# Kernel tuning notes

Measured on AMD Instinct MI355X. Metric: run time of the kernel, lower is better.

## Reference

```python
import jax, jax.numpy as jnp
import numpy as np
from jax import lax

EPS_BN = 1e-5
EPS_ADD = 1e-12


def _bn2d(x, g, b):
    # train-mode BatchNorm2d: stats over (N,H,W), biased variance
    m = x.mean(axis=(0, 2, 3), keepdims=True)
    v = x.var(axis=(0, 2, 3), keepdims=True)
    return (x - m) * lax.rsqrt(v + EPS_BN) * g[None, :, None, None] + b[None, :, None, None]


def _bn1d(x, g, b):
    # train-mode BatchNorm1d on [B,C,L]: stats over (N,L)
    m = x.mean(axis=(0, 2), keepdims=True)
    v = x.var(axis=(0, 2), keepdims=True)
    return (x - m) * lax.rsqrt(v + EPS_BN) * g[None, :, None] + b[None, :, None]


def _addw(w, a, b):
    wr = jax.nn.relu(w)
    wn = wr / (wr.sum() + EPS_ADD)
    return wn[0] * a + wn[1] * b


def setup_inputs() -> dict:
    key = jax.random.key(0)
    B, C, L = 16, 128, 16384
    H = 8
    ks = jax.random.split(key, 16)
    inp = {
        "x": jax.random.normal(ks[0], (B, C, L), dtype=jnp.float32),
        "dw_w": jax.random.normal(ks[1], (3, C, 1, 3, 3), dtype=jnp.float32) * 0.1,
        "bn2_g": jnp.ones((3, C), jnp.float32),
        "bn2_b": jnp.zeros((3, C), jnp.float32),
        "pw_w": jax.random.normal(ks[2], (3, C, C), dtype=jnp.float32) * 0.05,
        "pw_b": jax.random.normal(ks[3], (3, C), dtype=jnp.float32) * 0.02,
        "add_w": jnp.ones((2,), jnp.float32),
        "bn1_g": jnp.ones((C,), jnp.float32),
        "bn1_b": jnp.zeros((C,), jnp.float32),
        "W1": jax.random.normal(ks[4], (C, C // 4), dtype=jnp.float32) * 0.05,
        "b1": jnp.zeros((C // 4,), jnp.float32),
        "W2": jax.random.normal(ks[5], (C // 4, C), dtype=jnp.float32) * 0.05,
        "b2": jnp.zeros((C,), jnp.float32),
        "ffn_add_w": jnp.ones((2,), jnp.float32),
        "ffn_bn_g": jnp.ones((C,), jnp.float32),
        "ffn_bn_b": jnp.zeros((C,), jnp.float32),
        "heads": 8,
    }
    return inp


def reference(x, dw_w, bn2_g, bn2_b, pw_w, pw_b, add_w, bn1_g, bn1_b,
              W1, b1, W2, b2, ffn_add_w, ffn_bn_g, ffn_bn_b, heads):
    B, C, L = x.shape
    S = int(np.sqrt(L))  # static perfect-square side
    maps = x.reshape(B, C, S, S)

    # q (stride 1), k, v (stride 2) branches: depthwise3x3 -> BN2d -> pointwise1x1 -> GELU
    outs = []
    for i, st in enumerate((1, 2, 2)):
        y = lax.conv_general_dilated(
            maps, dw_w[i], window_strides=(st, st), padding=[(1, 1), (1, 1)],
            feature_group_count=C, dimension_numbers=("NCHW", "OIHW", "NCHW"))
        y = _bn2d(y, bn2_g[i], bn2_b[i])
        y = jnp.einsum("oc,bchw->bohw", pw_w[i], y) + pw_b[i][None, :, None, None]
        outs.append(jax.nn.gelu(y, approximate=False))
    q, k, v = outs

    def flat(t):  # [B,C,h,w] -> [B, n, C]
        return t.reshape(t.shape[0], t.shape[1], -1).transpose(0, 2, 1)

    q, k, v = flat(q), flat(k), flat(v)  # q: [B,L,C]; k,v: [B,L/4,C]
    dh = C // heads
    qh = q.reshape(B, -1, heads, dh)
    kh = k.reshape(B, -1, heads, dh)
    vh = v.reshape(B, -1, heads, dh)
    qs = jax.nn.softmax(qh, axis=-1)      # softmax over per-head channel dim
    ks_ = jax.nn.softmax(kh, axis=1)      # softmax over key sequence dim
    kv = jnp.einsum("bnhd,bnhe->bhde", ks_, vh)   # [B,H,dh,dh] tiny
    att = jnp.einsum("blhd,bhde->blhe", qs, kv)   # [B,L,H,dh]
    mhlsa = att.transpose(0, 2, 3, 1).reshape(B, C, L)  # concat heads on channel

    att_out = _bn1d(_addw(add_w, mhlsa, x), bn1_g, bn1_b)  # [B,C,L]

    # FFN on [B,L,C]
    f = jax.nn.gelu(jnp.einsum("blc,cf->blf", att_out.transpose(0, 2, 1), W1) + b1, approximate=False)
    f = jax.nn.gelu(jnp.einsum("blf,fc->blc", f, W2) + b2, approximate=False)
    out = _bn1d(_addw(ffn_add_w, f.transpose(0, 2, 1), att_out), ffn_bn_g, ffn_bn_b)
    return out
```

## Files before the change

kernel.cpp:

```cpp
#include <hip/hip_runtime.h>
#include <hip/hip_bf16.h>
#include <math.h>

#define BB 16
#define CC 128
#define LL 16384
#define SS 128
#define LK 4096
#define NHEAD 8
#define DH 16

typedef __attribute__((ext_vector_type(8))) short short8;
typedef __attribute__((ext_vector_type(4))) float f32x4;

__device__ __forceinline__ float gelu_f(float x) {
    return 0.5f * x * (1.0f + erff(x * 0.70710678118654752f));
}

__device__ __forceinline__ ushort f2bf(float f) {
    __hip_bfloat16 h = __float2bfloat16(f);
    return *(ushort*)&h;
}
__device__ __forceinline__ float bf2f(ushort u) {
    union { unsigned int i; float f; } x; x.i = ((unsigned int)u) << 16; return x.f;
}

__device__ __forceinline__ void block_reduce2(float& s1, float& s2) {
    #pragma unroll
    for (int off = 32; off; off >>= 1) {
        s1 += __shfl_down(s1, off);
        s2 += __shfl_down(s2, off);
    }
    __shared__ float red[2][4];
    int wid = threadIdx.x >> 6, lid = threadIdx.x & 63;
    if (lid == 0) { red[0][wid] = s1; red[1][wid] = s2; }
    __syncthreads();
    if (threadIdx.x == 0) {
        int nw = blockDim.x >> 6;
        float a = 0.f, b = 0.f;
        for (int i = 0; i < nw; i++) { a += red[0][i]; b += red[1][i]; }
        s1 = a; s2 = b;
    }
}

__global__ __launch_bounds__(256) void k_dw(const float* __restrict__ x,
        const float* __restrict__ dw_w,
        ushort* __restrict__ dwq, ushort* __restrict__ dwk, ushort* __restrict__ dwv,
        float* __restrict__ dwstats) {
    int bx = blockIdx.x;
    int cg = bx & 3;
    int oh = (bx >> 2) & 127;
    int b  = bx >> 9;
    __shared__ float xs[3][32][132];
    int tid = threadIdx.x;
    int cl  = tid >> 3;
    int owg = tid & 7;
    int ow0 = owg * 16;
    int c   = cg * 32 + cl;
    bool do_kv = ((oh & 1) == 0);

    float wq[9], wk[9], wv[9];
    const float* wp = dw_w + (size_t)c * 9;
    #pragma unroll
    for (int t = 0; t < 9; t++) wq[t] = wp[t];
    #pragma unroll
    for (int t = 0; t < 9; t++) wk[t] = wp[(size_t)CC * 9 + t];
    #pragma unroll
    for (int t = 0; t < 9; t++) wv[t] = wp[(size_t)2 * CC * 9 + t];

    for (int i = tid; i < 3 * 32 * 32; i += 256) {
        int r = i >> 10;
        int rem = i & 1023;
        int ch = rem >> 5;
        int f4 = rem & 31;
        int ih = oh - 1 + r;
        float4 v = make_float4(0.f, 0.f, 0.f, 0.f);
        if (ih >= 0 && ih < 128)
            v = *(const float4*)(x + ((size_t)b * CC + cg * 32 + ch) * (size_t)LL + ih * SS + f4 * 4);
        *(float4*)&xs[r][ch][f4 * 4] = v;
    }
    if (tid < 96) {
        int r = tid >> 5, ch = tid & 31;
        *(float4*)&xs[r][ch][128] = make_float4(0.f, 0.f, 0.f, 0.f);
    }
    __syncthreads();

    float aq[16], ak[8], av[8];
    #pragma unroll
    for (int j = 0; j < 16; j++) aq[j] = 0.f;
    #pragma unroll
    for (int j = 0; j < 8; j++) { ak[j] = 0.f; av[j] = 0.f; }

    #pragma unroll
    for (int r = 0; r < 3; r++) {
        const float* row = &xs[r][cl][0];
        float g[18];
        g[0] = owg ? row[ow0 - 1] : 0.f;
        float4 v0 = *(const float4*)&row[ow0];
        float4 v1 = *(const float4*)&row[ow0 + 4];
        float4 v2 = *(const float4*)&row[ow0 + 8];
        float4 v3 = *(const float4*)&row[ow0 + 12];
        g[1] = v0.x;  g[2] = v0.y;  g[3] = v0.z;  g[4] = v0.w;
        g[5] = v1.x;  g[6] = v1.y;  g[7] = v1.z;  g[8] = v1.w;
        g[9] = v2.x;  g[10] = v2.y; g[11] = v2.z; g[12] = v2.w;
        g[13] = v3.x; g[14] = v3.y; g[15] = v3.z; g[16] = v3.w;
        g[17] = row[ow0 + 16];
        float w0 = wq[3 * r], w1 = wq[3 * r + 1], w2 = wq[3 * r + 2];
        #pragma unroll
        for (int j = 0; j < 16; j++)
            aq[j] += w0 * g[j] + w1 * g[j + 1] + w2 * g[j + 2];
        if (do_kv) {
            float k0 = wk[3 * r], k1 = wk[3 * r + 1], k2 = wk[3 * r + 2];
            float x0 = wv[3 * r], x1 = wv[3 * r + 1], x2 = wv[3 * r + 2];
            #pragma unroll
            for (int j = 0; j < 8; j++) {
                ak[j] += k0 * g[2 * j] + k1 * g[2 * j + 1] + k2 * g[2 * j + 2];
                av[j] += x0 * g[2 * j] + x1 * g[2 * j + 1] + x2 * g[2 * j + 2];
            }
        }
    }

    ushort qb[16], kb16[8], vb16[8];
    {
        float s1 = 0.f, s2 = 0.f;
        #pragma unroll
        for (int j = 0; j < 16; j++) {
            qb[j] = f2bf(aq[j]);
            float fv = bf2f(qb[j]);
            s1 += fv; s2 += fv * fv;
        }
        #pragma unroll
        for (int m = 1; m <= 4; m <<= 1) {
            s1 += __shfl_xor(s1, m);
            s2 += __shfl_xor(s2, m);
        }
        if (owg == 0) {
            atomicAdd(&dwstats[(size_t)c * 2 + 0], s1);
            atomicAdd(&dwstats[(size_t)c * 2 + 1], s2);
        }
    }
    if (do_kv) {
        float t1 = 0.f, t2 = 0.f, u1 = 0.f, u2 = 0.f;
        #pragma unroll
        for (int j = 0; j < 8; j++) {
            kb16[j] = f2bf(ak[j]);
            float fk = bf2f(kb16[j]);
            t1 += fk; t2 += fk * fk;
            vb16[j] = f2bf(av[j]);
            float fv = bf2f(vb16[j]);
            u1 += fv; u2 += fv * fv;
        }
        #pragma unroll
        for (int m = 1; m <= 4; m <<= 1) {
            t1 += __shfl_xor(t1, m); t2 += __shfl_xor(t2, m);
            u1 += __shfl_xor(u1, m); u2 += __shfl_xor(u2, m);
        }
        if (owg == 0) {
            atomicAdd(&dwstats[((size_t)CC + c) * 2 + 0], t1);
            atomicAdd(&dwstats[((size_t)CC + c) * 2 + 1], t2);
            atomicAdd(&dwstats[((size_t)2 * CC + c) * 2 + 0], u1);
            atomicAdd(&dwstats[((size_t)2 * CC + c) * 2 + 1], u2);
        }
    }

    __syncthreads();
    unsigned int* qt = (unsigned int*)&xs[0][0][0];
    unsigned int* kt = qt + 64 * 33;
    unsigned int* vt = kt + 32 * 33;
    #pragma unroll
    for (int jp = 0; jp < 8; jp++)
        qt[(owg * 8 + jp) * 33 + cl] = (unsigned int)qb[2 * jp] | ((unsigned int)qb[2 * jp + 1] << 16);
    if (do_kv) {
        #pragma unroll
        for (int jp = 0; jp < 4; jp++) {
            kt[(owg * 4 + jp) * 33 + cl] = (unsigned int)kb16[2 * jp] | ((unsigned int)kb16[2 * jp + 1] << 16);
            vt[(owg * 4 + jp) * 33 + cl] = (unsigned int)vb16[2 * jp] | ((unsigned int)vb16[2 * jp + 1] << 16);
        }
    }
    __syncthreads();
    {
        ushort* qrow = dwq + (((size_t)b * 4 + cg) * LL + (size_t)oh * 128) * 32;
        #pragma unroll
        for (int cc = 0; cc < 2; cc++) {
            int i = tid + cc * 256;
            int p = i >> 2, c8 = (i & 3) * 8;
            int half = (p & 1) * 16;
            const unsigned int* src = qt + (p >> 1) * 33 + c8;
            union { ushort u[8]; float4 v; } pk;
            #pragma unroll
            for (int t2 = 0; t2 < 8; t2++) pk.u[t2] = (ushort)(src[t2] >> half);
            *(float4*)(qrow + (size_t)p * 32 + c8) = pk.v;
        }
    }
    if (do_kv) {
        int ohp = oh >> 1;
        size_t kvoff = (((size_t)b * 4 + cg) * LK + (size_t)ohp * 64) * 32;
        int p = tid >> 2, c8 = (tid & 3) * 8;
        int half = (p & 1) * 16;
        {
            const unsigned int* src = kt + (p >> 1) * 33 + c8;
            union { ushort u[8]; float4 v; } pk;
            #pragma unroll
            for (int t2 = 0; t2 < 8; t2++) pk.u[t2] = (ushort)(src[t2] >> half);
            *(float4*)(dwk + kvoff + (size_t)p * 32 + c8) = pk.v;
        }
        {
            const unsigned int* src = vt + (p >> 1) * 33 + c8;
            union { ushort u[8]; float4 v; } pk;
            #pragma unroll
            for (int t2 = 0; t2 < 8; t2++) pk.u[t2] = (ushort)(src[t2] >> half);
            *(float4*)(dwv + kvoff + (size_t)p * 32 + c8) = pk.v;
        }
    }
}

__global__ void k_finalize_dw(const float* __restrict__ stats, const float* __restrict__ pw_w,
                              const float* __restrict__ pw_b, const float* __restrict__ bn2_g,
                              const float* __restrict__ bn2_b,
                              ushort* __restrict__ effWb, float* __restrict__ effB) {
    int br = blockIdx.x >> 7;
    int o  = blockIdx.x & 127;
    int c  = threadIdx.x;
    float N = (br == 0) ? 262144.f : 65536.f;
    float s1 = stats[(br * CC + c) * 2 + 0];
    float s2 = stats[(br * CC + c) * 2 + 1];
    float m = s1 / N;
    float v = s2 / N - m * m;
    float sc = rsqrtf(v + 1e-5f);
    float A  = bn2_g[br * CC + c] * sc;
    float Bc = bn2_b[br * CC + c] - m * A;
    float w  = pw_w[((size_t)br * CC + o) * CC + c];
    effWb[((size_t)br * CC + o) * CC + c] = f2bf(w * A);
    float pb = w * Bc, dummy = 0.f;
    block_reduce2(pb, dummy);
    if (threadIdx.x == 0) effB[br * CC + o] = pw_b[br * CC + o] + pb;
}

__global__ __launch_bounds__(256, 3) void k_gemm_kv(const ushort* __restrict__ dwk,
        const ushort* __restrict__ dwv, const ushort* __restrict__ effWb,
        const float* __restrict__ effB, float* __restrict__ kbuf, float* __restrict__ vbuf) {
    __shared__ __align__(16) char raw[34816];
    short* Bs = (short*)raw;
    float* Sf = (float*)raw;
    int bx = blockIdx.x;
    int brv = bx >> 9;
    int b = (bx >> 5) & 15;
    int p0 = (bx & 31) * 128;
    const ushort* dw = brv ? dwv : dwk;
    const ushort* Wg = effWb + (size_t)(1 + brv) * CC * CC;
    int tid = threadIdx.x;
    for (int i = tid; i < 2048; i += 256) {
        int row = i >> 4; int f4 = i & 15;
        float4 v = *(const float4*)(Wg + (size_t)row * 128 + f4 * 8);
        *(float4*)&Bs[row * 136 + f4 * 8] = v;
    }
    __syncthreads();
    int w = tid >> 6, l = tid & 63;
    int m0 = w * 16;
    int la = l & 15, lb = l >> 4;
    f32x4 acc[2][8];
    #pragma unroll
    for (int i = 0; i < 2; i++)
        #pragma unroll
        for (int j = 0; j < 8; j++) acc[i][j] = (f32x4){0.f, 0.f, 0.f, 0.f};
    #pragma unroll
    for (int kt = 0; kt < 4; kt++) {
        short8 a0 = *(const short8*)(dw + (((size_t)b * 4 + kt) * LK + p0 + m0 + la) * 32 + lb * 8);
        short8 a1 = *(const short8*)(dw + (((size_t)b * 4 + kt) * LK + p0 + m0 + 64 + la) * 32 + lb * 8);
        int kb = kt * 32 + lb * 8;
        #pragma unroll
        for (int nt = 0; nt < 8; nt++) {
            short8 bf = *(const short8*)&Bs[(nt * 16 + la) * 136 + kb];
            acc[0][nt] = __builtin_amdgcn_mfma_f32_16x16x32_bf16(a0, bf, acc[0][nt], 0, 0, 0);
            acc[1][nt] = __builtin_amdgcn_mfma_f32_16x16x32_bf16(a1, bf, acc[1][nt], 0, 0, 0);
        }
    }
    float bias[8];
    #pragma unroll
    for (int nt = 0; nt < 8; nt++) bias[nt] = effB[(1 + brv) * CC + nt * 16 + la];
    float* outb = (brv ? vbuf : kbuf) + ((size_t)b * LK + p0) * CC;
    #pragma unroll
    for (int t = 0; t < 2; t++) {
        __syncthreads();
        #pragma unroll
        for (int nt = 0; nt < 8; nt++)
            #pragma unroll
            for (int i = 0; i < 4; i++) {
                float vv = acc[t][nt][i] + bias[nt];
                Sf[(m0 + lb * 4 + i) * 132 + nt * 16 + la] = gelu_f(vv);
            }
        __syncthreads();
        for (int i = tid; i < 2048; i += 256) {
            int r = i >> 5; int c4 = i & 31;
            *(float4*)(outb + (size_t)(t * 64 + r) * CC + c4 * 4) = *(const float4*)&Sf[r * 132 + c4 * 4];
        }
    }
}

__global__ void k_kv_accum(const float* __restrict__ k_buf, const float* __restrict__ v_buf,
                           float* __restrict__ kv_un, float* __restrict__ ssum) {
    int bx = blockIdx.x;
    int b = bx >> 5;
    int h = (bx >> 2) & 7;
    int sl = bx & 3;
    int n0 = sl * 1024;
    __shared__ float kch[64][16];
    __shared__ float vch[64][16];
    int tid = threadIdx.x;
    int d = tid >> 4, e = tid & 15;
    float acc = 0.f, ss = 0.f;
    for (int ch = 0; ch < 16; ch++) {
        int base = n0 + ch * 64;
        {
            int rr = tid >> 2, c4 = (tid & 3) * 4;
            const float* kp = k_buf + ((size_t)b * LK + base + rr) * CC + h * DH + c4;
            const float* vp = v_buf + ((size_t)b * LK + base + rr) * CC + h * DH + c4;
            float4 kf = *(const float4*)kp;
            float4 vf = *(const float4*)vp;
            kch[rr][c4+0] = __expf(kf.x); kch[rr][c4+1] = __expf(kf.y);
            kch[rr][c4+2] = __expf(kf.z); kch[rr][c4+3] = __expf(kf.w);
            vch[rr][c4+0] = vf.x; vch[rr][c4+1] = vf.y;
            vch[rr][c4+2] = vf.z; vch[rr][c4+3] = vf.w;
        }
        __syncthreads();
        #pragma unroll 8
        for (int rr = 0; rr < 64; rr++) {
            float ek = kch[rr][d];
            acc += ek * vch[rr][e];
            ss += ek;
        }
        __syncthreads();
    }
    atomicAdd(&kv_un[(((size_t)b * NHEAD + h) * DH + d) * DH + e], acc);
    if (e == 0) atomicAdd(&ssum[((size_t)b * NHEAD + h) * DH + d], ss);
}

__global__ void k_kv_div(const float* __restrict__ kv_un, const float* __restrict__ ssum,
                         float* __restrict__ kv) {
    int i = blockIdx.x * 256 + threadIdx.x;
    kv[i] = kv_un[i] / ssum[i >> 4];
}

__global__ __launch_bounds__(256, 3) void k_gemm_q(const ushort* __restrict__ dwq,
        const ushort* __restrict__ effWb, const float* __restrict__ effB,
        const float* __restrict__ kvb, const float* __restrict__ add_w,
        const float* __restrict__ x, float* __restrict__ y1) {
    __shared__ __align__(16) char raw[34816];
    short* Bs = (short*)raw;
    float* Sf = (float*)raw;
    __shared__ float kvs[2048];
    int bx = blockIdx.x;
    int b = bx >> 7;
    int p0 = (bx & 127) * 128;
    int tid = threadIdx.x;
    for (int i = tid; i < 512; i += 256)
        *(float4*)&kvs[i * 4] = *(const float4*)(kvb + (size_t)b * 2048 + i * 4);
    for (int i = tid; i < 2048; i += 256) {
        int row = i >> 4; int f4 = i & 15;
        float4 v = *(const float4*)(effWb + (size_t)row * 128 + f4 * 8);
        *(float4*)&Bs[row * 136 + f4 * 8] = v;
    }
    __syncthreads();
    int w = tid >> 6, l = tid & 63;
    int m0 = w * 16;
    int la = l & 15, lb = l >> 4;
    f32x4 acc[2][8];
    #pragma unroll
    for (int i = 0; i < 2; i++)
        #pragma unroll
        for (int j = 0; j < 8; j++) acc[i][j] = (f32x4){0.f, 0.f, 0.f, 0.f};
    #pragma unroll
    for (int kt = 0; kt < 4; kt++) {
        short8 a0 = *(const short8*)(dwq + (((size_t)b * 4 + kt) * LL + p0 + m0 + la) * 32 + lb * 8);
        short8 a1 = *(const short8*)(dwq + (((size_t)b * 4 + kt) * LL + p0 + m0 + 64 + la) * 32 + lb * 8);
        int kb = kt * 32 + lb * 8;
        #pragma unroll
        for (int nt = 0; nt < 8; nt++) {
            short8 bf = *(const short8*)&Bs[(nt * 16 + la) * 136 + kb];
            acc[0][nt] = __builtin_amdgcn_mfma_f32_16x16x32_bf16(a0, bf, acc[0][nt], 0, 0, 0);
            acc[1][nt] = __builtin_amdgcn_mfma_f32_16x16x32_bf16(a1, bf, acc[1][nt], 0, 0, 0);
        }
    }
    float bias[8];
    #pragma unroll
    for (int nt = 0; nt < 8; nt++) bias[nt] = effB[nt * 16 + la];
    float wa0 = add_w[0], wa1 = add_w[1];
    float r0 = fmaxf(wa0, 0.f), r1 = fmaxf(wa1, 0.f);
    float inv = 1.f / (r0 + r1 + 1e-12f);
    float wn0 = r0 * inv, wn1 = r1 * inv;
    #pragma unroll
    for (int t = 0; t < 2; t++) {
        __syncthreads();
        #pragma unroll
        for (int nt = 0; nt < 8; nt++)
            #pragma unroll
            for (int i = 0; i < 4; i++) {
                float vv = acc[t][nt][i] + bias[nt];
                Sf[(m0 + lb * 4 + i) * 133 + nt * 16 + la] = gelu_f(vv);
            }
        __syncthreads();
        int r64 = tid & 63;
        int hg = tid >> 6;
        int pact = t * 64 + r64;
        const float* xb = x + (size_t)b * CC * (size_t)LL + p0 + pact;
        float* yb = y1 + (size_t)b * CC * (size_t)LL + p0 + pact;
        #pragma unroll
        for (int hh = 0; hh < 2; hh++) {
            int h = hg * 2 + hh;
            float sv[16];
            float mx = -1e30f;
            #pragma unroll
            for (int d = 0; d < 16; d++) { sv[d] = Sf[r64 * 133 + h * 16 + d]; mx = fmaxf(mx, sv[d]); }
            float s = 0.f;
            #pragma unroll
            for (int d = 0; d < 16; d++) { sv[d] = __expf(sv[d] - mx); s += sv[d]; }
            float is = 1.f / s;
            #pragma unroll
            for (int e = 0; e < 16; e++) {
                float att = 0.f;
                #pragma unroll
                for (int d = 0; d < 16; d++) att += sv[d] * kvs[(h * 16 + d) * 16 + e];
                int c = h * 16 + e;
                yb[(size_t)c * LL] = wn0 * att * is + wn1 * xb[(size_t)c * LL];
            }
        }
    }
}

__global__ void k_chan_stats(const float* __restrict__ buf, float* __restrict__ stats) {
    int c = blockIdx.x >> 5;
    int s = blockIdx.x & 31;
    int b = s >> 1;
    int p0 = (s & 1) << 13;
    const float* src = buf + (size_t)b * (CC * (size_t)LL) + (size_t)c * LL + p0;
    float s1 = 0.f, s2 = 0.f;
    for (int i = threadIdx.x * 4; i < 8192; i += 1024) {
        float4 v = *(const float4*)(src + i);
        s1 += v.x + v.y + v.z + v.w;
        s2 += v.x * v.x + v.y * v.y + v.z * v.z + v.w * v.w;
    }
    block_reduce2(s1, s2);
    if (threadIdx.x == 0) {
        atomicAdd(&stats[c * 2 + 0], s1);
        atomicAdd(&stats[c * 2 + 1], s2);
    }
}

__global__ void k_fin1(const float* __restrict__ stats1, const float* __restrict__ bn1_g,
                       const float* __restrict__ bn1_b, const float* __restrict__ W1,
                       const float* __restrict__ b1, const float* __restrict__ W2,
                       float* __restrict__ A1B1, float* __restrict__ effW1,
                       float* __restrict__ effb1, float* __restrict__ W2T) {
    int t = threadIdx.x;
    const float N = 262144.f;
    float m = stats1[t * 2] / N;
    float v = stats1[t * 2 + 1] / N - m * m;
    float sc = rsqrtf(v + 1e-5f);
    float A = bn1_g[t] * sc;
    float Bc = bn1_b[t] - m * A;
    A1B1[t] = A; A1B1[128 + t] = Bc;
    __shared__ float Bs[128];
    Bs[t] = Bc;
    for (int j = 0; j < 32; j++) effW1[t * 32 + j] = W1[t * 32 + j] * A;
    for (int j = 0; j < 32; j++) W2T[t * 32 + j] = W2[j * 128 + t];
    __syncthreads();
    if (t < 32) {
        float s = b1[t];
        for (int c = 0; c < 128; c++) s += W1[c * 32 + t] * Bs[c];
        effb1[t] = s;
    }
}

__global__ __launch_bounds__(256) void k_ffn1(const float* __restrict__ y1,
        const float* __restrict__ effW1, const float* __restrict__ effb1,
        float* __restrict__ f1) {
    __shared__ float wl[4096];
    __shared__ float bl[32];
    int tid = threadIdx.x;
    for (int i = tid; i < 4096; i += 256) wl[i] = effW1[i];
    if (tid < 32) bl[tid] = effb1[tid];
    __syncthreads();
    int gp = blockIdx.x * 256 + tid;
    int b = gp >> 14, p = gp & 16383;
    const float* col = y1 + (size_t)b * (CC * (size_t)LL) + p;
    float acc[32];
    #pragma unroll
    for (int j = 0; j < 32; j++) acc[j] = bl[j];
    for (int c = 0; c < CC; c++) {
        float v = col[(size_t)c * LL];
        const float4* w4 = (const float4*)&wl[c * 32];
        #pragma unroll
        for (int i = 0; i < 8; i++) {
            float4 w = w4[i];
            acc[4*i+0] += w.x * v; acc[4*i+1] += w.y * v;
            acc[4*i+2] += w.z * v; acc[4*i+3] += w.w * v;
        }
    }
    float4* dst = (float4*)(f1 + (size_t)gp * 32);
    #pragma unroll
    for (int i = 0; i < 8; i++) {
        float4 o4;
        o4.x = gelu_f(acc[4*i+0]); o4.y = gelu_f(acc[4*i+1]);
        o4.z = gelu_f(acc[4*i+2]); o4.w = gelu_f(acc[4*i+3]);
        dst[i] = o4;
    }
}

__global__ __launch_bounds__(256) void k_ffn2(const float* __restrict__ f1,
        const float* __restrict__ W2T, const float* __restrict__ b2,
        const float* __restrict__ y1, const float* __restrict__ A1B1,
        const float* __restrict__ ffn_add_w, float* __restrict__ outb) {
    __shared__ float wl[4096];
    __shared__ float b2l[128];
    __shared__ float abl[256];
    int tid = threadIdx.x;
    for (int i = tid; i < 4096; i += 256) wl[i] = W2T[i];
    if (tid < 128) b2l[tid] = b2[tid];
    if (tid >= 128) abl[tid - 128] = A1B1[tid - 128];
    if (tid < 128) abl[128 + tid] = A1B1[128 + tid];
    __syncthreads();
    int gp = blockIdx.x * 256 + tid;
    int b = gp >> 14, p = gp & 16383;
    float f[32];
    {
        const float4* src = (const float4*)(f1 + (size_t)gp * 32);
        #pragma unroll
        for (int i = 0; i < 8; i++) {
            float4 v = src[i];
            f[4*i+0] = v.x; f[4*i+1] = v.y; f[4*i+2] = v.z; f[4*i+3] = v.w;
        }
    }
    float wa0 = ffn_add_w[0], wa1 = ffn_add_w[1];
    float r0 = fmaxf(wa0, 0.f), r1 = fmaxf(wa1, 0.f);
    float inv = 1.f / (r0 + r1 + 1e-12f);
    float wn0 = r0 * inv, wn1 = r1 * inv;
    const float* ycol = y1 + (size_t)b * (CC * (size_t)LL) + p;
    float* ocol = outb + (size_t)b * (CC * (size_t)LL) + p;
    for (int c = 0; c < CC; c++) {
        const float4* w4 = (const float4*)&wl[c * 32];
        float a = b2l[c];
        #pragma unroll
        for (int i = 0; i < 8; i++) {
            float4 w = w4[i];
            a += w.x * f[4*i+0] + w.y * f[4*i+1] + w.z * f[4*i+2] + w.w * f[4*i+3];
        }
        float f2 = gelu_f(a);
        float attv = ycol[(size_t)c * LL] * abl[c] + abl[128 + c];
        ocol[(size_t)c * LL] = wn0 * f2 + wn1 * attv;
    }
}

__global__ void k_fin2(const float* __restrict__ stats2, const float* __restrict__ g,
                       const float* __restrict__ bb, float* __restrict__ A2B2) {
    int t = threadIdx.x;
    const float N = 262144.f;
    float m = stats2[t * 2] / N;
    float v = stats2[t * 2 + 1] / N - m * m;
    float sc = rsqrtf(v + 1e-5f);
    float A = g[t] * sc;
    A2B2[t] = A;
    A2B2[128 + t] = bb[t] - m * A;
}

__global__ void k_norm(float* __restrict__ out, const float* __restrict__ A2B2) {
    size_t i = ((size_t)blockIdx.x * 256 + threadIdx.x) * 4;
    int c = (int)((i >> 14) & 127);
    float A = A2B2[c], Bc = A2B2[128 + c];
    float4 v = *(float4*)(out + i);
    v.x = v.x * A + Bc; v.y = v.y * A + Bc; v.z = v.z * A + Bc; v.w = v.w * A + Bc;
    *(float4*)(out + i) = v;
}

extern "C" void kernel_launch(void* const* d_in, const int* in_sizes, int n_in,
                              void* d_out, int out_size, void* d_ws, size_t ws_size,
                              hipStream_t stream) {
    const float* x        = (const float*)d_in[0];
    const float* dw_w     = (const float*)d_in[1];
    const float* bn2_g    = (const float*)d_in[2];
    const float* bn2_b    = (const float*)d_in[3];
    const float* pw_w     = (const float*)d_in[4];
    const float* pw_b     = (const float*)d_in[5];
    const float* add_w    = (const float*)d_in[6];
    const float* bn1_g    = (const float*)d_in[7];
    const float* bn1_b    = (const float*)d_in[8];
    const float* W1       = (const float*)d_in[9];
    const float* b1       = (const float*)d_in[10];
    const float* W2       = (const float*)d_in[11];
    const float* b2       = (const float*)d_in[12];
    const float* ffn_aw   = (const float*)d_in[13];
    const float* ffn_bn_g = (const float*)d_in[14];
    const float* ffn_bn_b = (const float*)d_in[15];

    float* w = (float*)d_ws;
    size_t off = 0;
    auto alloc = [&](size_t n) { float* p = w + off; off += n; return p; };
    float* dwstats = alloc(768);
    float* stats1  = alloc(256);
    float* stats2  = alloc(256);
    float* kv_un   = alloc(32768);
    float* ssum    = alloc(2048);
    size_t zero_bytes = off * sizeof(float);
    float* effWb_f = alloc(24576);
    float* effB    = alloc(384);
    float* kvb     = alloc(32768);
    float* A1B1    = alloc(256);
    float* effW1   = alloc(4096);
    float* effb1   = alloc(32);
    float* W2T     = alloc(4096);
    float* A2B2    = alloc(256);
    float* y1      = alloc((size_t)BB * CC * LL);
    float* kbuf    = alloc((size_t)BB * LK * CC);
    float* vbuf    = alloc((size_t)BB * LK * CC);
    float* dwq_f   = alloc((size_t)BB * LL * CC / 2);
    float* dwk_f   = alloc((size_t)BB * LK * CC / 2);
    float* dwv_f   = alloc((size_t)BB * LK * CC / 2);
    float* f1      = kbuf;
    (void)ws_size;

    ushort* effWb = (ushort*)effWb_f;
    ushort* dwq = (ushort*)dwq_f;
    ushort* dwk = (ushort*)dwk_f;
    ushort* dwv = (ushort*)dwv_f;
    float* outf = (float*)d_out;

    hipMemsetAsync(d_ws, 0, zero_bytes, stream);

    k_dw<<<8192, 256, 0, stream>>>(x, dw_w, dwq, dwk, dwv, dwstats);
    k_finalize_dw<<<384, 128, 0, stream>>>(dwstats, pw_w, pw_b, bn2_g, bn2_b, effWb, effB);
    k_gemm_kv<<<1024, 256, 0, stream>>>(dwk, dwv, effWb, effB, kbuf, vbuf);
    k_kv_accum<<<512, 256, 0, stream>>>(kbuf, vbuf, kv_un, ssum);
    k_kv_div<<<128, 256, 0, stream>>>(kv_un, ssum, kvb);
    k_gemm_q<<<2048, 256, 0, stream>>>(dwq, effWb, effB, kvb, add_w, x, y1);
    k_chan_stats<<<4096, 256, 0, stream>>>(y1, stats1);
    k_fin1<<<1, 128, 0, stream>>>(stats1, bn1_g, bn1_b, W1, b1, W2, A1B1, effW1, effb1, W2T);
    k_ffn1<<<1024, 256, 0, stream>>>(y1, effW1, effb1, f1);
    k_ffn2<<<1024, 256, 0, stream>>>(f1, W2T, b2, y1, A1B1, ffn_aw, outf);
    k_chan_stats<<<4096, 256, 0, stream>>>(outf, stats2);
    k_fin2<<<1, 128, 0, stream>>>(stats2, ffn_bn_g, ffn_bn_b, A2B2);
    k_norm<<<32768, 256, 0, stream>>>(outf, A2B2);
}
```

Before: 783.3 us.

## Fuse K/V GEMM with KV accumulation and fold BN1 stats into Q GEMM

The K and V pointwise GEMMs are merged into one kernel that computes exp(K) and accumulates exp(K)^T V and the exp sums directly into shared memory per block, then issues atomic adds to global. This drops the fp32 k/v buffers and the separate accumulation kernel. The Q GEMM epilogue now also accumulates per-channel sum and sum of squares through wave shuffles and atomics, which removes one full channel-stats pass over y1. The costs are more registers (two accumulator sets, occupancy hint lowered to 2), many shared-memory atomics, and an extra 64 per-thread stat registers in the Q kernel.

```diff
diff --git a/kernel.cpp b/kernel.cpp
--- a/kernel.cpp
+++ b/kernel.cpp
@@ -236,103 +236,122 @@
     if (threadIdx.x == 0) effB[br * CC + o] = pw_b[br * CC + o] + pb;
 }
 
-__global__ __launch_bounds__(256, 3) void k_gemm_kv(const ushort* __restrict__ dwk,
+__global__ __launch_bounds__(256, 2) void k_kv_fused(const ushort* __restrict__ dwk,
         const ushort* __restrict__ dwv, const ushort* __restrict__ effWb,
-        const float* __restrict__ effB, float* __restrict__ kbuf, float* __restrict__ vbuf) {
+        const float* __restrict__ effB, float* __restrict__ kv_un, float* __restrict__ ssum) {
     __shared__ __align__(16) char raw[34816];
     short* Bs = (short*)raw;
-    float* Sf = (float*)raw;
+    float* Sv = (float*)raw;
+    __shared__ float kvblk[NHEAD][DH][DH];
+    __shared__ float ssblk[NHEAD][DH];
     int bx = blockIdx.x;
-    int brv = bx >> 9;
-    int b = (bx >> 5) & 15;
+    int b = bx >> 5;
     int p0 = (bx & 31) * 128;
-    const ushort* dw = brv ? dwv : dwk;
-    const ushort* Wg = effWb + (size_t)(1 + brv) * CC * CC;
     int tid = threadIdx.x;
-    for (int i = tid; i < 2048; i += 256) {
-        int row = i >> 4; int f4 = i & 15;
-        float4 v = *(const float4*)(Wg + (size_t)row * 128 + f4 * 8);
-        *(float4*)&Bs[row * 136 + f4 * 8] = v;
+    for (int i = tid; i < 2048; i += 256) ((float*)kvblk)[i] = 0.f;
+    if (tid < 128) ((float*)ssblk)[tid] = 0.f;
+    {
+        const ushort* Wv = effWb + (size_t)2 * CC * CC;
+        for (int i = tid; i < 2048; i += 256) {
+            int row = i >> 4; int f4 = i & 15;
+            float4 v = *(const float4*)(Wv + (size_t)row * 128 + f4 * 8);
+            *(float4*)&Bs[row * 136 + f4 * 8] = v;
+        }
     }
     __syncthreads();
     int w = tid >> 6, l = tid & 63;
     int m0 = w * 16;
     int la = l & 15, lb = l >> 4;
-    f32x4 acc[2][8];
+    f32x4 accv[2][8], acck[2][8];
     #pragma unroll
     for (int i = 0; i < 2; i++)
         #pragma unroll
-        for (int j = 0; j < 8; j++) acc[i][j] = (f32x4){0.f, 0.f, 0.f, 0.f};
+        for (int j = 0; j < 8; j++) {
+            accv[i][j] = (f32x4){0.f, 0.f, 0.f, 0.f};
+            acck[i][j] = (f32x4){0.f, 0.f, 0.f, 0.f};
+        }
     #pragma unroll
     for (int kt = 0; kt < 4; kt++) {
-        short8 a0 = *(const short8*)(dw + (((size_t)b * 4 + kt) * LK + p0 + m0 + la) * 32 + lb * 8);
-        short8 a1 = *(const short8*)(dw + (((size_t)b * 4 + kt) * LK + p0 + m0 + 64 + la) * 32 + lb * 8);
+        short8 a0 = *(const short8*)(dwv + (((size_t)b * 4 + kt) * LK + p0 + m0 + la) * 32 + lb * 8);
+        short8 a1 = *(const short8*)(dwv + (((size_t)b * 4 + kt) * LK + p0 + m0 + 64 + la) * 32 + lb * 8);
         int kb = kt * 32 + lb * 8;
         #pragma unroll
         for (int nt = 0; nt < 8; nt++) {
             short8 bf = *(const short8*)&Bs[(nt * 16 + la) * 136 + kb];
-            acc[0][nt] = __builtin_amdgcn_mfma_f32_16x16x32_bf16(a0, bf, acc[0][nt], 0, 0, 0);
-            acc[1][nt] = __builtin_amdgcn_mfma_f32_16x16x32_bf16(a1, bf, acc[1][nt], 0, 0, 0);
-        }
-    }
-    float bias[8];
-    #pragma unroll
-    for (int nt = 0; nt < 8; nt++) bias[nt] = effB[(1 + brv) * CC + nt * 16 + la];
-    float* outb = (brv ? vbuf : kbuf) + ((size_t)b * LK + p0) * CC;
+            accv[0][nt] = __builtin_amdgcn_mfma_f32_16x16x32_bf16(a0, bf, accv[0][nt], 0, 0, 0);
+            accv[1][nt] = __builtin_amdgcn_mfma_f32_16x16x32_bf16(a1, bf, accv[1][nt], 0, 0, 0);
+        }
+    }
+    __syncthreads();
+    {
+        const ushort* Wk = effWb + (size_t)1 * CC * CC;
+        for (int i = tid; i < 2048; i += 256) {
+            int row = i >> 4; int f4 = i & 15;
+            float4 v = *(const float4*)(Wk + (size_t)row * 128 + f4 * 8);
+            *(float4*)&Bs[row * 136 + f4 * 8] = v;
+        }
+    }
+    __syncthreads();
+    #pragma unroll
+    for (int kt = 0; kt < 4; kt++) {
+        short8 a0 = *(const short8*)(dwk + (((size_t)b * 4 + kt) * LK + p0 + m0 + la) * 32 + lb * 8);
+        short8 a1 = *(const short8*)(dwk + (((size_t)b * 4 + kt) * LK + p0 + m0 + 64 + la) * 32 + lb * 8);
+        int kb = kt * 32 + lb * 8;
+        #pragma unroll
+        for (int nt = 0; nt < 8; nt++) {
+            short8 bf = *(const short8*)&Bs[(nt * 16 + la) * 136 + kb];
+            acck[0][nt] = __builtin_amdgcn_mfma_f32_16x16x32_bf16(a0, bf, acck[0][nt], 0, 0, 0);
+            acck[1][nt] = __builtin_amdgcn_mfma_f32_16x16x32_bf16(a1, bf, acck[1][nt], 0, 0, 0);
+        }
+    }
+    float biasv[8], biask[8];
+    #pragma unroll
+    for (int nt = 0; nt < 8; nt++) {
+        biask[nt] = effB[1 * CC + nt * 16 + la];
+        biasv[nt] = effB[2 * CC + nt * 16 + la];
+    }
     #pragma unroll
     for (int t = 0; t < 2; t++) {
         __syncthreads();
         #pragma unroll
         for (int nt = 0; nt < 8; nt++)
             #pragma unroll
+            for (int i = 0; i < 4; i++)
+                Sv[(m0 + lb * 4 + i) * 132 + nt * 16 + la] = gelu_f(accv[t][nt][i] + biasv[nt]);
+        __syncthreads();
+        #pragma unroll
+        for (int nt = 0; nt < 8; nt++) {
+            float kv16[16];
+            #pragma unroll
+            for (int e = 0; e < 16; e++) kv16[e] = 0.f;
+            float se = 0.f;
+            #pragma unroll
             for (int i = 0; i < 4; i++) {
-                float vv = acc[t][nt][i] + bias[nt];
-                Sf[(m0 + lb * 4 + i) * 132 + nt * 16 + la] = gelu_f(vv);
+                float ek = __expf(gelu_f(acck[t][nt][i] + biask[nt]));
+                se += ek;
+                const float4* vr4 = (const float4*)&Sv[(m0 + lb * 4 + i) * 132 + nt * 16];
+                #pragma unroll
+                for (int q4 = 0; q4 < 4; q4++) {
+                    float4 vv = vr4[q4];
+                    kv16[4 * q4 + 0] += ek * vv.x;
+                    kv16[4 * q4 + 1] += ek * vv.y;
+                    kv16[4 * q4 + 2] += ek * vv.z;
+                    kv16[4 * q4 + 3] += ek * vv.w;
+                }
             }
-        __syncthreads();
-        for (int i = tid; i < 2048; i += 256) {
-            int r = i >> 5; int c4 = i & 31;
-            *(float4*)(outb + (size_t)(t * 64 + r) * CC + c4 * 4) = *(const float4*)&Sf[r * 132 + c4 * 4];
-        }
-    }
-}
-
-__global__ void k_kv_accum(const float* __restrict__ k_buf, const float* __restrict__ v_buf,
-                           float* __restrict__ kv_un, float* __restrict__ ssum) {
-    int bx = blockIdx.x;
-    int b = bx >> 5;
-    int h = (bx >> 2) & 7;
-    int sl = bx & 3;
-    int n0 = sl * 1024;
-    __shared__ float kch[64][16];
-    __shared__ float vch[64][16];
-    int tid = threadIdx.x;
-    int d = tid >> 4, e = tid & 15;
-    float acc = 0.f, ss = 0.f;
-    for (int ch = 0; ch < 16; ch++) {
-        int base = n0 + ch * 64;
-        {
-            int rr = tid >> 2, c4 = (tid & 3) * 4;
-            const float* kp = k_buf + ((size_t)b * LK + base + rr) * CC + h * DH + c4;
-            const float* vp = v_buf + ((size_t)b * LK + base + rr) * CC + h * DH + c4;
-            float4 kf = *(const float4*)kp;
-            float4 vf = *(const float4*)vp;
-            kch[rr][c4+0] = __expf(kf.x); kch[rr][c4+1] = __expf(kf.y);
-            kch[rr][c4+2] = __expf(kf.z); kch[rr][c4+3] = __expf(kf.w);
-            vch[rr][c4+0] = vf.x; vch[rr][c4+1] = vf.y;
-            vch[rr][c4+2] = vf.z; vch[rr][c4+3] = vf.w;
-        }
-        __syncthreads();
-        #pragma unroll 8
-        for (int rr = 0; rr < 64; rr++) {
-            float ek = kch[rr][d];
-            acc += ek * vch[rr][e];
-            ss += ek;
-        }
-        __syncthreads();
-    }
-    atomicAdd(&kv_un[(((size_t)b * NHEAD + h) * DH + d) * DH + e], acc);
-    if (e == 0) atomicAdd(&ssum[((size_t)b * NHEAD + h) * DH + d], ss);
+            #pragma unroll
+            for (int e = 0; e < 16; e++) atomicAdd(&kvblk[nt][la][e], kv16[e]);
+            atomicAdd(&ssblk[nt][la], se);
+        }
+    }
+    __syncthreads();
+    for (int i = tid; i < 2048; i += 256) {
+        int h = i >> 8;
+        atomicAdd(&kv_un[(size_t)b * 2048 + i], ((float*)kvblk)[i]);
+        (void)h;
+    }
+    if (tid < 128)
+        atomicAdd(&ssum[(size_t)b * 128 + tid], ((float*)ssblk)[tid]);
 }
 
 __global__ void k_kv_div(const float* __restrict__ kv_un, const float* __restrict__ ssum,
@@ -344,7 +363,7 @@
 __global__ __launch_bounds__(256, 3) void k_gemm_q(const ushort* __restrict__ dwq,
         const ushort* __restrict__ effWb, const float* __restrict__ effB,
         const float* __restrict__ kvb, const float* __restrict__ add_w,
-        const float* __restrict__ x, float* __restrict__ y1) {
+        const float* __restrict__ x, float* __restrict__ y1, float* __restrict__ stats1) {
     __shared__ __align__(16) char raw[34816];
     short* Bs = (short*)raw;
     float* Sf = (float*)raw;
@@ -388,6 +407,9 @@
     float r0 = fmaxf(wa0, 0.f), r1 = fmaxf(wa1, 0.f);
     float inv = 1.f / (r0 + r1 + 1e-12f);
     float wn0 = r0 * inv, wn1 = r1 * inv;
+    float ls1[32], ls2[32];
+    #pragma unroll
+    for (int ce = 0; ce < 32; ce++) { ls1[ce] = 0.f; ls2[ce] = 0.f; }
     #pragma unroll
     for (int t = 0; t < 2; t++) {
         __syncthreads();
@@ -421,9 +443,28 @@
                 #pragma unroll
                 for (int d = 0; d < 16; d++) att += sv[d] * kvs[(h * 16 + d) * 16 + e];
                 int c = h * 16 + e;
-                yb[(size_t)c * LL] = wn0 * att * is + wn1 * xb[(size_t)c * LL];
+                float yv = wn0 * att * is + wn1 * xb[(size_t)c * LL];
+                yb[(size_t)c * LL] = yv;
+                ls1[hh * 16 + e] += yv;
+                ls2[hh * 16 + e] += yv * yv;
             }
         }
+    }
+    float rs1 = 0.f, rs2 = 0.f;
+    #pragma unroll
+    for (int ce = 0; ce < 32; ce++) {
+        float a = ls1[ce], bb2 = ls2[ce];
+        #pragma unroll
+        for (int off = 32; off; off >>= 1) {
+            a += __shfl_xor(a, off);
+            bb2 += __shfl_xor(bb2, off);
+        }
+        if (l == ce) { rs1 = a; rs2 = bb2; }
+    }
+    if (l < 32) {
+        int c = (tid >> 6) * 32 + l;
+        atomicAdd(&stats1[c * 2 + 0], rs1);
+        atomicAdd(&stats1[c * 2 + 1], rs2);
     }
 }
 
@@ -609,12 +650,10 @@
     float* W2T     = alloc(4096);
     float* A2B2    = alloc(256);
     float* y1      = alloc((size_t)BB * CC * LL);
-    float* kbuf    = alloc((size_t)BB * LK * CC);
-    float* vbuf    = alloc((size_t)BB * LK * CC);
+    float* f1      = alloc((size_t)BB * LL * 32);
     float* dwq_f   = alloc((size_t)BB * LL * CC / 2);
     float* dwk_f   = alloc((size_t)BB * LK * CC / 2);
     float* dwv_f   = alloc((size_t)BB * LK * CC / 2);
-    float* f1      = kbuf;
     (void)ws_size;
 
     ushort* effWb = (ushort*)effWb_f;
@@ -627,11 +666,9 @@
 
     k_dw<<<8192, 256, 0, stream>>>(x, dw_w, dwq, dwk, dwv, dwstats);
     k_finalize_dw<<<384, 128, 0, stream>>>(dwstats, pw_w, pw_b, bn2_g, bn2_b, effWb, effB);
-    k_gemm_kv<<<1024, 256, 0, stream>>>(dwk, dwv, effWb, effB, kbuf, vbuf);
-    k_kv_accum<<<512, 256, 0, stream>>>(kbuf, vbuf, kv_un, ssum);
+    k_kv_fused<<<512, 256, 0, stream>>>(dwk, dwv, effWb, effB, kv_un, ssum);
     k_kv_div<<<128, 256, 0, stream>>>(kv_un, ssum, kvb);
-    k_gemm_q<<<2048, 256, 0, stream>>>(dwq, effWb, effB, kvb, add_w, x, y1);
-    k_chan_stats<<<4096, 256, 0, stream>>>(y1, stats1);
+    k_gemm_q<<<2048, 256, 0, stream>>>(dwq, effWb, effB, kvb, add_w, x, y1, stats1);
     k_fin1<<<1, 128, 0, stream>>>(stats1, bn1_g, bn1_b, W1, b1, W2, A1B1, effW1, effb1, W2T);
     k_ffn1<<<1024, 256, 0, stream>>>(y1, effW1, effb1, f1);
     k_ffn2<<<1024, 256, 0, stream>>>(f1, W2T, b2, y1, A1B1, ffn_aw, outf);
```

Result: slower. 998.9 us (+27.5%).
